# Kernel optimization log

Measured on AMD Instinct MI355X. Metric: run time of the kernel, lower is better.

The kernel has to match this reference:

```python
import jax, jax.numpy as jnp
import numpy as np
from jax import lax

DIM = 1024
N_EXPERTS = 64
TOPK = 8
ROUTE_SCALE = 1.0
B = 262144


def setup_inputs() -> dict:
    key = jax.random.key(0)
    kx, kw, kb = jax.random.split(key, 3)
    x = jax.random.normal(kx, (B, DIM), dtype=jnp.float32)
    # nn.Linear(dim, n_experts): weight [E, dim], bias [E]
    bound = 1.0 / np.sqrt(DIM)
    W = jax.random.uniform(kw, (N_EXPERTS, DIM), minval=-bound, maxval=bound, dtype=jnp.float32)
    b = jax.random.uniform(kb, (N_EXPERTS,), minval=-bound, maxval=bound, dtype=jnp.float32)
    return {"x": x, "W": W, "b": b}


def reference(x, W, b):
    # Router linear: [B, dim] x [dim, E] -> [B, E]
    scores = jnp.einsum("bd,ed->be", x, W) + b
    # score_func == 'softmax' (computed in fp32 as in the torch module)
    probs = jax.nn.softmax(scores.astype(jnp.float32), axis=-1)
    # topk + gather (topk values ARE the gathered original scores)
    weights, indices = lax.top_k(probs, TOPK)            # [B, topk] each
    weights = (weights * ROUTE_SCALE).astype(x.dtype)
    # training-time expert usage histogram (replaces the per-expert python loop)
    expert_usage_count = jnp.zeros((N_EXPERTS,), dtype=jnp.float32).at[indices.reshape(-1)].add(1.0)
    total_tokens = jnp.float32(B * TOPK)
    return weights, indices, expert_usage_count, total_tokens
```

## Files before the change

kernel.cpp:

```cpp
#include <hip/hip_runtime.h>
#include <math.h>

#define NTOK   262144
#define DIM    1024
#define NEXP   64
#define TOPK   8
#define WROWS  32
#define ROWS   128
#define BLK    256
#define BK     32
#define NKC    (DIM / BK)
#define BUFSZ  4096
#define SLICE  (3 * BUFSZ)

#define OFF_IDX ((size_t)NTOK * TOPK)
#define OFF_USE (2 * (size_t)NTOK * TOPK)
#define OFF_TOT (OFF_USE + NEXP)

typedef __attribute__((ext_vector_type(8))) short bf16x8;
typedef __attribute__((ext_vector_type(4))) float f32x4;

union FragU { bf16x8 v; unsigned int u[4]; };

__device__ __forceinline__ bf16x8 pack_bf16(float4 a, float4 b) {
    FragU r;
    r.u[0] = (__float_as_uint(a.x) >> 16) | (__float_as_uint(a.y) & 0xFFFF0000u);
    r.u[1] = (__float_as_uint(a.z) >> 16) | (__float_as_uint(a.w) & 0xFFFF0000u);
    r.u[2] = (__float_as_uint(b.x) >> 16) | (__float_as_uint(b.y) & 0xFFFF0000u);
    r.u[3] = (__float_as_uint(b.z) >> 16) | (__float_as_uint(b.w) & 0xFFFF0000u);
    return r.v;
}

__global__ __launch_bounds__(256) void gate_prep_kernel(const float* __restrict__ W,
                                                        unsigned short* __restrict__ wf,
                                                        float* __restrict__ out) {
    int idx = blockIdx.x * 256 + threadIdx.x;
    int j    = idx & 7;
    int lane = (idx >> 3) & 63;
    int nt   = (idx >> 9) & 3;
    int kc   = idx >> 11;
    int fq = lane >> 4, fr = lane & 15;
    float v = W[(size_t)(nt * 16 + fr) * DIM + kc * BK + fq * 8 + j];
    unsigned int u = __float_as_uint(v);
    u += 0x7FFFu + ((u >> 16) & 1u);
    wf[idx] = (unsigned short)(u >> 16);

    if (blockIdx.x == 0) {
        if (threadIdx.x < NEXP) out[OFF_USE + threadIdx.x] = 0.0f;
        if (threadIdx.x == NEXP) out[OFF_TOT] = (float)((size_t)NTOK * TOPK);
    }
}

__global__ __launch_bounds__(BLK, 3) void gate_kernel(const float* __restrict__ x,
                                                      const unsigned short* __restrict__ wf,
                                                      const float* __restrict__ bias,
                                                      float* __restrict__ out) {
    __shared__ __align__(16) char smem[4 * SLICE];
    __shared__ float hist[NEXP];

    const int tid  = threadIdx.x;
    const int w    = tid >> 6;
    const int lane = tid & 63;
    const int fq   = lane >> 4;
    const int fr   = lane & 15;
    const size_t rowBase = (size_t)blockIdx.x * ROWS;

    if (tid < NEXP) hist[tid] = 0.0f;

    char* myslice = smem + w * SLICE;

    const char* xb = (const char*)(x + (rowBase + (size_t)w * WROWS) * DIM);
    const char* src[4];
#pragma unroll
    for (int i = 0; i < 4; i++) {
        int flat = i * 64 + lane;
        int row = flat >> 3;
        int u = (flat & 7) ^ (row & 7);
        src[i] = xb + (size_t)row * (DIM * 4) + u * 16;
    }

#define STAGE(BUF, kc)                                                            \
    do {                                                                          \
        _Pragma("unroll")                                                         \
        for (int i_ = 0; i_ < 4; i_++)                                            \
            __builtin_amdgcn_global_load_lds(                                     \
                (const __attribute__((address_space(1))) unsigned int*)(src[i_] + (kc) * 128), \
                (__attribute__((address_space(3))) unsigned int*)(myslice + (BUF) * BUFSZ + i_ * 1024), \
                16, 0, 2 );                  \
    } while (0)

    int aslot[2][2];
#pragma unroll
    for (int mt = 0; mt < 2; mt++)
#pragma unroll
        for (int h = 0; h < 2; h++)
            aslot[mt][h] = (mt * 16 + fr) * 8 + (((fq * 2 + h) ^ fr) & 7);

    const bf16x8* wfv = (const bf16x8*)wf;

    f32x4 acc[2][4] = {};
    bf16x8 bcur[4];

#pragma unroll
    for (int nt = 0; nt < 4; nt++) bcur[nt] = wfv[(size_t)nt * 64 + lane];
    __builtin_amdgcn_sched_barrier(0);
    STAGE(0, 0);
    STAGE(1, 1);

#define GSTEP(kc, BUF, SBUF, MODE)                                                \
    {                                                                             \
        bf16x8 bnext[4];                                                          \
        if ((MODE) >= 1) {                                                        \
            _Pragma("unroll")                                                     \
            for (int nt = 0; nt < 4; nt++)                                        \
                bnext[nt] = wfv[(size_t)(((kc) + 1) * 4 + nt) * 64 + lane];       \
            __builtin_amdgcn_sched_barrier(0);                                    \
        }                                                                         \
        if ((MODE) == 2) STAGE(SBUF, (kc) + 2);                                   \
        if ((MODE) == 2)      asm volatile("s_waitcnt vmcnt(12)" ::: "memory");   \
        else if ((MODE) == 1) asm volatile("s_waitcnt vmcnt(8)" ::: "memory");    \
        else                  asm volatile("s_waitcnt vmcnt(0)" ::: "memory");    \
        __builtin_amdgcn_sched_barrier(0);                                        \
        const float4* xt = (const float4*)(myslice + (BUF) * BUFSZ);              \
        _Pragma("unroll")                                                         \
        for (int mt = 0; mt < 2; mt++) {                                          \
            bf16x8 af = pack_bf16(xt[aslot[mt][0]], xt[aslot[mt][1]]);            \
            _Pragma("unroll")                                                     \
            for (int nt = 0; nt < 4; nt++)                                        \
                acc[mt][nt] = __builtin_amdgcn_mfma_f32_16x16x32_bf16(af, bcur[nt], acc[mt][nt], 0, 0, 0); \
        }                                                                         \
        if ((MODE) >= 1) {                                                        \
            _Pragma("unroll")                                                     \
            for (int nt = 0; nt < 4; nt++) bcur[nt] = bnext[nt];                  \
        }                                                                         \
    }

#pragma unroll 1
    for (int t = 0; t < 10; t++) {
        GSTEP(3 * t,     0, 2, 2);
        GSTEP(3 * t + 1, 1, 0, 2);
        GSTEP(3 * t + 2, 2, 1, 2);
    }
    GSTEP(30, 0, 0, 1);
    GSTEP(31, 1, 0, 0);

    float* sw = (float*)myslice;
    float bv[4];
#pragma unroll
    for (int nt = 0; nt < 4; nt++) bv[nt] = bias[nt * 16 + fr];
#pragma unroll
    for (int mt = 0; mt < 2; mt++) {
        int mbase = mt * 16 + fq * 4;
#pragma unroll
        for (int nt = 0; nt < 4; nt++) {
            int n = nt * 16 + fr;
#pragma unroll
            for (int r = 0; r < 4; r++)
                sw[(mbase + r) * 65 + n] = acc[mt][nt][r] + bv[nt];
        }
    }
    __syncthreads();

    if (tid < ROWS) {
        const float* rp = (const float*)(smem + (tid >> 5) * SLICE) + (tid & 31) * 65;

        float tv[8]; int ti[8];
#pragma unroll
        for (int k = 0; k < 8; k++) { tv[k] = -1e30f; ti[k] = 0; }

#pragma unroll 4
        for (int e = 0; e < NEXP; e++) {
            float s = rp[e];
#pragma unroll
            for (int k = 7; k >= 1; k--) {
                bool up   = s > tv[k - 1];
                bool here = s > tv[k];
                float nv = up ? tv[k - 1] : (here ? s : tv[k]);
                int   ni = up ? ti[k - 1] : (here ? e : ti[k]);
                tv[k] = nv; ti[k] = ni;
            }
            bool c0 = s > tv[0];
            ti[0] = c0 ? e : ti[0];
            tv[0] = c0 ? s : tv[0];
        }
        float m = tv[0];

        float sum = 0.0f;
#pragma unroll 8
        for (int e = 0; e < NEXP; e++) sum += __expf(rp[e] - m);
        float rinv = 1.0f / sum;

        float wv_[8];
#pragma unroll
        for (int k = 0; k < 8; k++) wv_[k] = __expf(tv[k] - m) * rinv;

        size_t ro = (rowBase + tid) * TOPK;
        *(float4*)(out + ro)     = make_float4(wv_[0], wv_[1], wv_[2], wv_[3]);
        *(float4*)(out + ro + 4) = make_float4(wv_[4], wv_[5], wv_[6], wv_[7]);
        *(float4*)(out + OFF_IDX + ro)     = make_float4((float)ti[0], (float)ti[1], (float)ti[2], (float)ti[3]);
        *(float4*)(out + OFF_IDX + ro + 4) = make_float4((float)ti[4], (float)ti[5], (float)ti[6], (float)ti[7]);
#pragma unroll
        for (int k = 0; k < 8; k++) atomicAdd(&hist[ti[k]], 1.0f);
    }
    __syncthreads();
    if (tid < NEXP) atomicAdd(&out[OFF_USE + tid], hist[tid]);
}

extern "C" void kernel_launch(void* const* d_in, const int* in_sizes, int n_in,
                              void* d_out, int out_size, void* d_ws, size_t ws_size,
                              hipStream_t stream) {
    const float* x    = (const float*)d_in[0];
    const float* W    = (const float*)d_in[1];
    const float* bias = (const float*)d_in[2];
    float* out = (float*)d_out;
    unsigned short* wf = (unsigned short*)d_ws;

    gate_prep_kernel<<<256, 256, 0, stream>>>(W, wf, out);
    gate_kernel<<<NTOK / ROWS, BLK, 0, stream>>>(x, wf, bias, out);
}
```

Baseline: 245.3 us.

## Double K-slab per stage, halve block size, and stagger slab start per wave

Each pipeline stage now loads a 64-wide K slab (16 slabs instead of 32 steps), so each wave issues twice as many async global-to-LDS loads and runs twice as many MFMAs per wait. The block shrinks to 2 waves covering 64 rows, which doubles the grid. The K iteration start is rotated by block and wave index so concurrent waves touch different address ranges and weight fragments. This aims to cut per-step wait/barrier overhead and spread memory traffic, at the cost of more LDS per wave and more registers for the doubled B fragments.

```diff
diff --git a/kernel.cpp b/kernel.cpp
--- a/kernel.cpp
+++ b/kernel.cpp
@@ -6,11 +6,10 @@
 #define NEXP   64
 #define TOPK   8
 #define WROWS  32
-#define ROWS   128
-#define BLK    256
-#define BK     32
-#define NKC    (DIM / BK)
-#define BUFSZ  4096
+#define ROWS   64
+#define BLK    128
+#define NSLAB  16
+#define BUFSZ  8192
 #define SLICE  (3 * BUFSZ)
 
 #define OFF_IDX ((size_t)NTOK * TOPK)
@@ -40,7 +39,7 @@
     int nt   = (idx >> 9) & 3;
     int kc   = idx >> 11;
     int fq = lane >> 4, fr = lane & 15;
-    float v = W[(size_t)(nt * 16 + fr) * DIM + kc * BK + fq * 8 + j];
+    float v = W[(size_t)(nt * 16 + fr) * DIM + kc * 32 + fq * 8 + j];
     unsigned int u = __float_as_uint(v);
     u += 0x7FFFu + ((u >> 16) & 1u);
     wf[idx] = (unsigned short)(u >> 16);
@@ -51,11 +50,11 @@
     }
 }
 
-__global__ __launch_bounds__(BLK, 3) void gate_kernel(const float* __restrict__ x,
-                                                      const unsigned short* __restrict__ wf,
-                                                      const float* __restrict__ bias,
-                                                      float* __restrict__ out) {
-    __shared__ __align__(16) char smem[4 * SLICE];
+__global__ __launch_bounds__(BLK) void gate_kernel(const float* __restrict__ x,
+                                                   const unsigned short* __restrict__ wf,
+                                                   const float* __restrict__ bias,
+                                                   float* __restrict__ out) {
+    __shared__ __align__(16) char smem[2 * SLICE];
     __shared__ float hist[NEXP];
 
     const int tid  = threadIdx.x;
@@ -70,79 +69,90 @@
     char* myslice = smem + w * SLICE;
 
     const char* xb = (const char*)(x + (rowBase + (size_t)w * WROWS) * DIM);
-    const char* src[4];
-#pragma unroll
-    for (int i = 0; i < 4; i++) {
+    const char* src[8];
+#pragma unroll
+    for (int i = 0; i < 8; i++) {
         int flat = i * 64 + lane;
-        int row = flat >> 3;
-        int u = (flat & 7) ^ (row & 7);
+        int row = flat >> 4;
+        int u = (flat & 15) ^ (row & 15);
         src[i] = xb + (size_t)row * (DIM * 4) + u * 16;
     }
 
-#define STAGE(BUF, kc)                                                            \
+#define STAGE(BUF, sp)                                                            \
     do {                                                                          \
         _Pragma("unroll")                                                         \
-        for (int i_ = 0; i_ < 4; i_++)                                            \
+        for (int i_ = 0; i_ < 8; i_++)                                            \
             __builtin_amdgcn_global_load_lds(                                     \
-                (const __attribute__((address_space(1))) unsigned int*)(src[i_] + (kc) * 128), \
+                (const __attribute__((address_space(1))) unsigned int*)(src[i_] + (size_t)(sp) * 256), \
                 (__attribute__((address_space(3))) unsigned int*)(myslice + (BUF) * BUFSZ + i_ * 1024), \
-                16, 0, 2 );                  \
+                16, 0, 2 );                                \
     } while (0)
 
-    int aslot[2][2];
-#pragma unroll
-    for (int mt = 0; mt < 2; mt++)
-#pragma unroll
-        for (int h = 0; h < 2; h++)
-            aslot[mt][h] = (mt * 16 + fr) * 8 + (((fq * 2 + h) ^ fr) & 7);
+    int aslot[2][2][2];
+#pragma unroll
+    for (int kk = 0; kk < 2; kk++)
+#pragma unroll
+        for (int mt = 0; mt < 2; mt++)
+#pragma unroll
+            for (int h = 0; h < 2; h++)
+                aslot[kk][mt][h] = (mt * 16 + fr) * 16 + ((kk * 8 + fq * 2 + h) ^ fr);
 
     const bf16x8* wfv = (const bf16x8*)wf;
 
     f32x4 acc[2][4] = {};
-    bf16x8 bcur[4];
-
-#pragma unroll
-    for (int nt = 0; nt < 4; nt++) bcur[nt] = wfv[(size_t)nt * 64 + lane];
+    bf16x8 bcur[8];
+
+    const int sp0 = ((int)blockIdx.x + (w << 3)) & 15;
+
+#pragma unroll
+    for (int f = 0; f < 8; f++) bcur[f] = wfv[(size_t)(sp0 * 8 + f) * 64 + lane];
     __builtin_amdgcn_sched_barrier(0);
-    STAGE(0, 0);
-    STAGE(1, 1);
-
-#define GSTEP(kc, BUF, SBUF, MODE)                                                \
+    STAGE(0, sp0);
+    STAGE(1, (sp0 + 1) & 15);
+
+#define GSTEP(SP, BUF, SBUF, MODE)                                                \
     {                                                                             \
-        bf16x8 bnext[4];                                                          \
+        const int sp_ = (SP);                                                     \
+        bf16x8 bnext[8];                                                          \
         if ((MODE) >= 1) {                                                        \
+            const int sn_ = (sp_ + 1) & 15;                                       \
             _Pragma("unroll")                                                     \
-            for (int nt = 0; nt < 4; nt++)                                        \
-                bnext[nt] = wfv[(size_t)(((kc) + 1) * 4 + nt) * 64 + lane];       \
+            for (int f = 0; f < 8; f++)                                           \
+                bnext[f] = wfv[(size_t)(sn_ * 8 + f) * 64 + lane];                \
             __builtin_amdgcn_sched_barrier(0);                                    \
         }                                                                         \
-        if ((MODE) == 2) STAGE(SBUF, (kc) + 2);                                   \
-        if ((MODE) == 2)      asm volatile("s_waitcnt vmcnt(12)" ::: "memory");   \
-        else if ((MODE) == 1) asm volatile("s_waitcnt vmcnt(8)" ::: "memory");    \
+        if ((MODE) == 2) STAGE(SBUF, (sp_ + 2) & 15);                             \
+        if ((MODE) == 2)      asm volatile("s_waitcnt vmcnt(24)" ::: "memory");   \
+        else if ((MODE) == 1) asm volatile("s_waitcnt vmcnt(16)" ::: "memory");   \
         else                  asm volatile("s_waitcnt vmcnt(0)" ::: "memory");    \
         __builtin_amdgcn_sched_barrier(0);                                        \
         const float4* xt = (const float4*)(myslice + (BUF) * BUFSZ);              \
         _Pragma("unroll")                                                         \
-        for (int mt = 0; mt < 2; mt++) {                                          \
-            bf16x8 af = pack_bf16(xt[aslot[mt][0]], xt[aslot[mt][1]]);            \
+        for (int kk = 0; kk < 2; kk++) {                                          \
             _Pragma("unroll")                                                     \
-            for (int nt = 0; nt < 4; nt++)                                        \
-                acc[mt][nt] = __builtin_amdgcn_mfma_f32_16x16x32_bf16(af, bcur[nt], acc[mt][nt], 0, 0, 0); \
+            for (int mt = 0; mt < 2; mt++) {                                      \
+                bf16x8 af = pack_bf16(xt[aslot[kk][mt][0]], xt[aslot[kk][mt][1]]); \
+                _Pragma("unroll")                                                 \
+                for (int nt = 0; nt < 4; nt++)                                    \
+                    acc[mt][nt] = __builtin_amdgcn_mfma_f32_16x16x32_bf16(af, bcur[kk * 4 + nt], acc[mt][nt], 0, 0, 0); \
+            }                                                                     \
         }                                                                         \
         if ((MODE) >= 1) {                                                        \
             _Pragma("unroll")                                                     \
-            for (int nt = 0; nt < 4; nt++) bcur[nt] = bnext[nt];                  \
+            for (int f = 0; f < 8; f++) bcur[f] = bnext[f];                       \
         }                                                                         \
     }
 
 #pragma unroll 1
-    for (int t = 0; t < 10; t++) {
-        GSTEP(3 * t,     0, 2, 2);
-        GSTEP(3 * t + 1, 1, 0, 2);
-        GSTEP(3 * t + 2, 2, 1, 2);
-    }
-    GSTEP(30, 0, 0, 1);
-    GSTEP(31, 1, 0, 0);
+    for (int t = 0; t < 4; t++) {
+        GSTEP((sp0 + 3 * t) & 15,     0, 2, 2);
+        GSTEP((sp0 + 3 * t + 1) & 15, 1, 0, 2);
+        GSTEP((sp0 + 3 * t + 2) & 15, 2, 1, 2);
+    }
+    GSTEP((sp0 + 12) & 15, 0, 2, 2);
+    GSTEP((sp0 + 13) & 15, 1, 0, 2);
+    GSTEP((sp0 + 14) & 15, 2, 0, 1);
+    GSTEP((sp0 + 15) & 15, 0, 0, 0);
 
     float* sw = (float*)myslice;
     float bv[4];
```

New measurement: 277.4 us. +13.1%, slower.
